# Kernel optimization log

Hardware: AMD Instinct MI355X
Metric: run time of the kernel (lower is better)

The kernel has to match this reference:

```python
import jax, jax.numpy as jnp
import numpy as np

N = 100000   # nodes
E = 1600000  # edges
P = 16       # num_properties
H = 64       # hidden_dim
EPS = 1e-12  # F.normalize eps


def _lin_params(key, din, dout):
    return (jax.random.normal(key, (din, dout), jnp.float32) / np.sqrt(din),
            jnp.zeros((dout,), jnp.float32))


def _mlp(x, W1, b1, W2, b2):
    # MLP(in, out, hidden_layers=[H]): Linear -> ReLU -> Linear
    return jnp.maximum(x @ W1 + b1, 0.0) @ W2 + b2


def setup_inputs() -> dict:
    key = jax.random.key(0)
    ks = jax.random.split(key, 12)
    h = jax.random.normal(ks[0], (N, P), jnp.float32)
    x = jax.random.normal(ks[1], (N, 3), jnp.float32)
    edge_index = jax.random.randint(ks[2], (2, E), 0, N, jnp.int64)
    emb_W, emb_b = _lin_params(ks[3], P, H)
    eW1, eb1 = _lin_params(ks[4], 2 * H + 1, H)
    eW2, eb2 = _lin_params(ks[5], H, H)
    nW1, nb1 = _lin_params(ks[6], 2 * H, H)
    nW2, nb2 = _lin_params(ks[7], H, H)
    wW1, wb1 = _lin_params(ks[8], H, H)
    wW2, wb2 = _lin_params(ks[9], H, 1)
    return {"h": h, "x": x, "edge_index": edge_index,
            "emb_W": emb_W, "emb_b": emb_b,
            "eW1": eW1, "eb1": eb1, "eW2": eW2, "eb2": eb2,
            "nW1": nW1, "nb1": nb1, "nW2": nW2, "nb2": nb2,
            "wW1": wW1, "wb1": wb1, "wW2": wW2, "wb2": wb2}


def reference(h, x, edge_index, emb_W, emb_b, eW1, eb1, eW2, eb2,
              nW1, nb1, nW2, nb2, wW1, wb1, wW2, wb2):
    row, col = edge_index[0], edge_index[1]
    h = h @ emb_W + emb_b  # [N,H] node embedding

    rel_pos = x[row] - x[col]                               # [E,3]
    rel_dist = jnp.sum(rel_pos ** 2, axis=-1, keepdims=True)  # [E,1]
    rel_theta = jnp.arctan2(rel_pos[:, 1], rel_pos[:, 0])
    rel_phi = jnp.arctan2(rel_pos[:, 2],
                          jnp.sqrt(rel_pos[:, 0] ** 2 + rel_pos[:, 1] ** 2))
    rel_pos_spin2 = rel_dist * jnp.stack(
        [jnp.cos(2 * rel_theta), jnp.sin(2 * rel_theta), rel_phi], axis=1)  # [E,3]

    # single layer (num_layers=1; original code only executable in this config)
    edge_inputs = jnp.concatenate([h[row], h[col], rel_dist], axis=-1)  # [E,2H+1]
    edge_feat = _mlp(edge_inputs, eW1, eb1, eW2, eb2)                   # [E,H]
    agg = jax.ops.segment_sum(edge_feat, row, num_segments=N)           # [N,H]
    h = h + _mlp(jnp.concatenate([h, agg], axis=-1), nW1, nb1, nW2, nb2)

    w = _mlp(edge_feat, wW1, wb1, wW2, wb2)              # [E,1]
    rel_scaled = rel_pos_spin2[:, None, :] * w[:, :, None]  # [E,1,3]
    v_sum = jax.ops.segment_sum(rel_scaled, row, num_segments=N)  # [N,1,3]
    cnt = jax.ops.segment_sum(jnp.ones((E,), jnp.float32), row, num_segments=N)
    v = v_sum / jnp.maximum(cnt, 1.0)[:, None, None]     # scatter-mean

    v = v[:, :2]  # slice along dim 1 (faithful to torch v[:, :2])
    norm = jnp.linalg.norm(v, axis=-1, keepdims=True)
    v = v / jnp.maximum(norm, EPS)  # F.normalize(p=2, dim=-1)
    return (h, x, v)
```

## Files before the change

kernel.cpp:

```cpp
#include <hip/hip_runtime.h>
#include <math.h>

#define NN 100000
#define EE 1600000
#define NBLK_SCAN 256
#define CHUNK ((NN + NBLK_SCAN - 1) / NBLK_SCAN)

typedef __attribute__((ext_vector_type(8))) short bf16x8;
typedef __attribute__((ext_vector_type(4))) float f32x4;

__device__ __forceinline__ ushort f2bf(float x) {
    uint u = __builtin_bit_cast(uint, x);
    u += 0x7fffu + ((u >> 16) & 1u);
    return (ushort)(u >> 16);
}
__device__ __forceinline__ float bf2f(ushort u) {
    uint v = ((uint)u) << 16;
    return __builtin_bit_cast(float, v);
}

__global__ __launch_bounds__(256) void embed_kernel(
    const float* __restrict__ h, const float* __restrict__ embW,
    const float* __restrict__ embB, ushort* __restrict__ hembb)
{
    int t = blockIdx.x * 256 + threadIdx.x;
    int n = t >> 6;
    int j = t & 63;
    if (n >= NN) return;
    float acc = embB[j];
#pragma unroll
    for (int k = 0; k < 16; ++k)
        acc = fmaf(h[n * 16 + k], embW[k * 64 + j], acc);
    hembb[n * 64 + j] = f2bf(acc);
}

__global__ __launch_bounds__(256) void hist_kernel(
    const int* __restrict__ ei, int* __restrict__ hist)
{
    for (int e = blockIdx.x * 256 + threadIdx.x; e < EE; e += gridDim.x * 256)
        atomicAdd(&hist[ei[e]], 1);
}

__global__ __launch_bounds__(256) void scan_a(const int* __restrict__ hist, int* __restrict__ bsum)
{
    __shared__ int red[256];
    const int b = blockIdx.x, t = threadIdx.x;
    const int start = b * CHUNK, end = min(NN, start + CHUNK);
    int s = 0;
    for (int i = start + t; i < end; i += 256) s += hist[i];
    red[t] = s; __syncthreads();
    for (int k = 128; k > 0; k >>= 1) { if (t < k) red[t] += red[t + k]; __syncthreads(); }
    if (t == 0) bsum[b] = red[0];
}

__global__ void scan_b(const int* __restrict__ bsum, int* __restrict__ boff)
{
    if (threadIdx.x == 0) {
        int acc = 0;
        for (int i = 0; i < NBLK_SCAN; ++i) { boff[i] = acc; acc += bsum[i]; }
    }
}

__global__ __launch_bounds__(256) void scan_c(
    const int* __restrict__ hist, const int* __restrict__ boff,
    int* __restrict__ csr, int* __restrict__ cursor)
{
    __shared__ int lds[CHUNK];
    const int b = blockIdx.x, t = threadIdx.x;
    const int start = b * CHUNK, end = min(NN, start + CHUNK), n = end - start;
    for (int i = t; i < n; i += 256) lds[i] = hist[start + i];
    __syncthreads();
    if (t == 0) {
        int acc = boff[b];
        for (int i = 0; i < n; ++i) { int v = lds[i]; lds[i] = acc; acc += v; }
        if (end == NN) csr[NN] = acc;
    }
    __syncthreads();
    for (int i = t; i < n; i += 256) { csr[start + i] = lds[i]; cursor[start + i] = lds[i]; }
}

__global__ __launch_bounds__(256) void scatter_kernel(
    const int* __restrict__ ei, int* __restrict__ cursor, int2* __restrict__ srt)
{
    for (int e = blockIdx.x * 256 + threadIdx.x; e < EE; e += gridDim.x * 256) {
        const int row = ei[e];
        const int p = atomicAdd(&cursor[row], 1);
        srt[p] = make_int2(row, ei[EE + e]);
    }
}

__global__ __launch_bounds__(512, 2) void edge_kernel(
    const ushort* __restrict__ hembb, const float* __restrict__ x,
    const int2* __restrict__ srt,
    const float* __restrict__ eW1, const float* __restrict__ eb1,
    const float* __restrict__ eW2, const float* __restrict__ eb2,
    const float* __restrict__ wW1, const float* __restrict__ wb1,
    const float* __restrict__ wW2, const float* __restrict__ wb2,
    float* __restrict__ agg, float* __restrict__ vsum)
{
    __shared__ ushort sS[8][2560];
    __shared__ float  sScal[8][16][4];

    const int tid = threadIdx.x;
    const int wave = tid >> 6, lane = tid & 63;
    const int l15 = lane & 15, g = lane >> 4;

    bf16x8 W1f[4][4], W2f[2][4], WVf[2][4];
#pragma unroll
    for (int kc = 0; kc < 4; ++kc)
#pragma unroll
        for (int t = 0; t < 4; ++t) {
            bf16x8 f;
#pragma unroll
            for (int b = 0; b < 8; ++b) {
                int k = kc * 32 + g * 8 + b;
                f[b] = (short)f2bf(eW1[k * 64 + t * 16 + l15]);
            }
            W1f[kc][t] = f;
        }
#pragma unroll
    for (int kc = 0; kc < 2; ++kc)
#pragma unroll
        for (int t = 0; t < 4; ++t) {
            bf16x8 f, fv;
#pragma unroll
            for (int b = 0; b < 8; ++b) {
                int s = kc * 32 + g * 8 + b;
                int j = (s >> 2) + (s & 3) * 16;
                f[b]  = (short)f2bf(eW2[j * 64 + t * 16 + l15]);
                fv[b] = (short)f2bf(wW1[j * 64 + t * 16 + l15]);
            }
            W2f[kc][t] = f; WVf[kc][t] = fv;
        }
    float b1v[4], b2v[4], wb1v[4], w2v[4], w128v[4];
#pragma unroll
    for (int t = 0; t < 4; ++t) {
        b1v[t]   = eb1[t * 16 + l15];
        b2v[t]   = eb2[t * 16 + l15];
        wb1v[t]  = wb1[t * 16 + l15];
        w2v[t]   = wW2[t * 16 + l15];
        w128v[t] = eW1[128 * 64 + t * 16 + l15];
    }
    const float wb2v = wb2[0];

    ushort* Xl = sS[wave];
    ushort* T1 = sS[wave];
    ushort* EF = sS[wave] + 1280;

    const int base = (blockIdx.x * 8 + wave) * 400;

    float carry = 0.f, carryv = 0.f;
    int cur_row = -1;

    for (int bt = 0; bt < 25; ++bt) {
        const int ebase = base + bt * 16;

        int rowv = 0, colv = 0;
        if (lane < 16) {
            const int2 rc = srt[ebase + lane];
            rowv = rc.x; colv = rc.y;
            const float dx = x[rowv * 3 + 0] - x[colv * 3 + 0];
            const float dy = x[rowv * 3 + 1] - x[colv * 3 + 1];
            const float dz = x[rowv * 3 + 2] - x[colv * 3 + 2];
            const float r2 = dx * dx + dy * dy;
            const float rdv = r2 + dz * dz;
            const float inv = (r2 > 0.f) ? (1.f / r2) : 0.f;
            const float c2  = (r2 > 0.f) ? ((dx * dx - dy * dy) * inv) : 1.f;
            const float sn2 = 2.f * dx * dy * inv;
            const float phi = atan2f(dz, sqrtf(r2));
            float4 sc = {rdv, rdv * c2, rdv * sn2, rdv * phi};
            *(float4*)&sScal[wave][lane][0] = sc;
        }

        uint gv[16];
#pragma unroll
        for (int e = 0; e < 16; ++e) {
            const int re = __shfl(rowv, e);
            const int ce = __shfl(colv, e);
            const int node = (lane < 32) ? re : ce;
            gv[e] = *(const uint*)&hembb[(size_t)node * 64 + (lane & 31) * 2];
        }
#pragma unroll
        for (int e = 0; e < 16; ++e)
            *(uint*)&Xl[e * 144 + (lane & 31) * 2 + ((lane < 32) ? 0 : 64)] = gv[e];

        f32x4 acc[4];
#pragma unroll
        for (int t = 0; t < 4; ++t) acc[t] = (f32x4){b1v[t], b1v[t], b1v[t], b1v[t]};
#pragma unroll
        for (int kc = 0; kc < 4; ++kc) {
            bf16x8 a = *(const bf16x8*)&Xl[l15 * 144 + kc * 32 + g * 8];
#pragma unroll
            for (int t = 0; t < 4; ++t)
                acc[t] = __builtin_amdgcn_mfma_f32_16x16x32_bf16(a, W1f[kc][t], acc[t], 0, 0, 0);
        }
#pragma unroll
        for (int r = 0; r < 4; ++r) {
            const float rd_r = sScal[wave][g * 4 + r][0];
#pragma unroll
            for (int t = 0; t < 4; ++t) acc[t][r] = fmaf(rd_r, w128v[t], acc[t][r]);
        }
#pragma unroll
        for (int r = 0; r < 4; ++r) {
            const float v0 = fmaxf(acc[0][r], 0.f), v1 = fmaxf(acc[1][r], 0.f);
            const float v2 = fmaxf(acc[2][r], 0.f), v3 = fmaxf(acc[3][r], 0.f);
            uint2 p;
            p.x = (uint)f2bf(v0) | ((uint)f2bf(v1) << 16);
            p.y = (uint)f2bf(v2) | ((uint)f2bf(v3) << 16);
            *(uint2*)&T1[(g * 4 + r) * 80 + l15 * 4] = p;
        }

        f32x4 acc2[4];
#pragma unroll
        for (int t = 0; t < 4; ++t) acc2[t] = (f32x4){b2v[t], b2v[t], b2v[t], b2v[t]};
#pragma unroll
        for (int kc = 0; kc < 2; ++kc) {
            bf16x8 a = *(const bf16x8*)&T1[l15 * 80 + kc * 32 + g * 8];
#pragma unroll
            for (int t = 0; t < 4; ++t)
                acc2[t] = __builtin_amdgcn_mfma_f32_16x16x32_bf16(a, W2f[kc][t], acc2[t], 0, 0, 0);
        }
#pragma unroll
        for (int r = 0; r < 4; ++r) {
            uint2 p;
            p.x = (uint)f2bf(acc2[0][r]) | ((uint)f2bf(acc2[1][r]) << 16);
            p.y = (uint)f2bf(acc2[2][r]) | ((uint)f2bf(acc2[3][r]) << 16);
            *(uint2*)&EF[(g * 4 + r) * 80 + l15 * 4] = p;
        }

        f32x4 acc3[4];
#pragma unroll
        for (int t = 0; t < 4; ++t) acc3[t] = (f32x4){wb1v[t], wb1v[t], wb1v[t], wb1v[t]};
#pragma unroll
        for (int kc = 0; kc < 2; ++kc) {
            bf16x8 a = *(const bf16x8*)&EF[l15 * 80 + kc * 32 + g * 8];
#pragma unroll
            for (int t = 0; t < 4; ++t)
                acc3[t] = __builtin_amdgcn_mfma_f32_16x16x32_bf16(a, WVf[kc][t], acc3[t], 0, 0, 0);
        }
        float wfin[4];
#pragma unroll
        for (int r = 0; r < 4; ++r) {
            float p = fmaxf(acc3[0][r], 0.f) * w2v[0];
            p = fmaf(fmaxf(acc3[1][r], 0.f), w2v[1], p);
            p = fmaf(fmaxf(acc3[2][r], 0.f), w2v[2], p);
            p = fmaf(fmaxf(acc3[3][r], 0.f), w2v[3], p);
            wfin[r] = p;
        }
#pragma unroll
        for (int m = 1; m < 16; m <<= 1) {
#pragma unroll
            for (int r = 0; r < 4; ++r) wfin[r] += __shfl_xor(wfin[r], m);
        }
#pragma unroll
        for (int r = 0; r < 4; ++r) wfin[r] += wb2v;

#pragma unroll
        for (int e = 0; e < 16; ++e) {
            const int row_e = __shfl(rowv, e);
            const float efv = bf2f(EF[e * 80 + l15 * 4 + g]);
            const float wE = __shfl(wfin[e & 3], (e >> 2) * 16);
            if (row_e != cur_row) {
                if (cur_row >= 0) {
                    unsafeAtomicAdd(&agg[(size_t)cur_row * 64 + lane], carry);
                    if (lane < 3) unsafeAtomicAdd(&vsum[cur_row * 4 + lane], carryv);
                }
                cur_row = row_e; carry = 0.f; carryv = 0.f;
            }
            carry += efv;
            if (lane < 3) carryv = fmaf(sScal[wave][e][1 + lane], wE, carryv);
        }
    }
    if (cur_row >= 0) {
        unsafeAtomicAdd(&agg[(size_t)cur_row * 64 + lane], carry);
        if (lane < 3) unsafeAtomicAdd(&vsum[cur_row * 4 + lane], carryv);
    }
}

__global__ __launch_bounds__(256, 2) void node_kernel(
    const ushort* __restrict__ hembb, const float* __restrict__ agg,
    const float* __restrict__ nW1, const float* __restrict__ nb1,
    const float* __restrict__ nW2, const float* __restrict__ nb2,
    const float* __restrict__ vsum, const int* __restrict__ csr,
    float* __restrict__ outh, float* __restrict__ outv)
{
    __shared__ ushort sT1[4][16 * 80];

    const int tid = threadIdx.x;
    const int wave = tid >> 6, lane = tid & 63;
    const int l15 = lane & 15, g = lane >> 4;

    bf16x8 W1f[4][4], W2f[2][4];
#pragma unroll
    for (int kc = 0; kc < 4; ++kc)
#pragma unroll
        for (int t = 0; t < 4; ++t) {
            bf16x8 f;
#pragma unroll
            for (int b = 0; b < 8; ++b) {
                int k = kc * 32 + g * 8 + b;
                f[b] = (short)f2bf(nW1[k * 64 + t * 16 + l15]);
            }
            W1f[kc][t] = f;
        }
#pragma unroll
    for (int kc = 0; kc < 2; ++kc)
#pragma unroll
        for (int t = 0; t < 4; ++t) {
            bf16x8 f;
#pragma unroll
            for (int b = 0; b < 8; ++b) {
                int s = kc * 32 + g * 8 + b;
                int j = (s >> 2) + (s & 3) * 16;
                f[b] = (short)f2bf(nW2[j * 64 + t * 16 + l15]);
            }
            W2f[kc][t] = f;
        }
    float b1v[4], b2v[4];
#pragma unroll
    for (int t = 0; t < 4; ++t) { b1v[t] = nb1[t * 16 + l15]; b2v[t] = nb2[t * 16 + l15]; }

    ushort* T1 = sT1[wave];
    const int nwaves = gridDim.x * 4;
    const int ntiles = NN / 16;

    for (int tile = blockIdx.x * 4 + wave; tile < ntiles; tile += nwaves) {
        const int nb = tile * 16;

        f32x4 acc[4];
#pragma unroll
        for (int t = 0; t < 4; ++t) acc[t] = (f32x4){b1v[t], b1v[t], b1v[t], b1v[t]};
#pragma unroll
        for (int kc = 0; kc < 2; ++kc) {
            bf16x8 a = *(const bf16x8*)&hembb[(size_t)(nb + l15) * 64 + kc * 32 + g * 8];
#pragma unroll
            for (int t = 0; t < 4; ++t)
                acc[t] = __builtin_amdgcn_mfma_f32_16x16x32_bf16(a, W1f[kc][t], acc[t], 0, 0, 0);
        }
#pragma unroll
        for (int kc = 2; kc < 4; ++kc) {
            const float4 f0 = *(const float4*)&agg[(size_t)(nb + l15) * 64 + (kc - 2) * 32 + g * 8];
            const float4 f1 = *(const float4*)&agg[(size_t)(nb + l15) * 64 + (kc - 2) * 32 + g * 8 + 4];
            bf16x8 a;
            a[0] = (short)f2bf(f0.x); a[1] = (short)f2bf(f0.y);
            a[2] = (short)f2bf(f0.z); a[3] = (short)f2bf(f0.w);
            a[4] = (short)f2bf(f1.x); a[5] = (short)f2bf(f1.y);
            a[6] = (short)f2bf(f1.z); a[7] = (short)f2bf(f1.w);
#pragma unroll
            for (int t = 0; t < 4; ++t)
                acc[t] = __builtin_amdgcn_mfma_f32_16x16x32_bf16(a, W1f[kc][t], acc[t], 0, 0, 0);
        }
#pragma unroll
        for (int r = 0; r < 4; ++r) {
            const float v0 = fmaxf(acc[0][r], 0.f), v1 = fmaxf(acc[1][r], 0.f);
            const float v2 = fmaxf(acc[2][r], 0.f), v3 = fmaxf(acc[3][r], 0.f);
            uint2 p;
            p.x = (uint)f2bf(v0) | ((uint)f2bf(v1) << 16);
            p.y = (uint)f2bf(v2) | ((uint)f2bf(v3) << 16);
            *(uint2*)&T1[(g * 4 + r) * 80 + l15 * 4] = p;
        }

        f32x4 acc2[4];
#pragma unroll
        for (int t = 0; t < 4; ++t) acc2[t] = (f32x4){b2v[t], b2v[t], b2v[t], b2v[t]};
#pragma unroll
        for (int kc = 0; kc < 2; ++kc) {
            bf16x8 a = *(const bf16x8*)&T1[l15 * 80 + kc * 32 + g * 8];
#pragma unroll
            for (int t = 0; t < 4; ++t)
                acc2[t] = __builtin_amdgcn_mfma_f32_16x16x32_bf16(a, W2f[kc][t], acc2[t], 0, 0, 0);
        }
#pragma unroll
        for (int r = 0; r < 4; ++r) {
#pragma unroll
            for (int t = 0; t < 4; ++t) {
                const size_t idx = (size_t)(nb + g * 4 + r) * 64 + t * 16 + l15;
                outh[idx] = bf2f(hembb[idx]) + acc2[t][r];
            }
        }

        if (g == 0) {
            const int n = nb + l15;
            const float c = fmaxf((float)(csr[n + 1] - csr[n]), 1.f);
            const float4 vs = *(const float4*)&vsum[n * 4];
            const float a0 = vs.x / c, a1 = vs.y / c, a2 = vs.z / c;
            const float nrm = fmaxf(sqrtf(a0 * a0 + a1 * a1 + a2 * a2), 1e-12f);
            outv[n * 3 + 0] = a0 / nrm;
            outv[n * 3 + 1] = a1 / nrm;
            outv[n * 3 + 2] = a2 / nrm;
        }
    }
}

extern "C" void kernel_launch(void* const* d_in, const int* in_sizes, int n_in,
                              void* d_out, int out_size, void* d_ws, size_t ws_size,
                              hipStream_t stream)
{
    const float* h    = (const float*)d_in[0];
    const float* x    = (const float*)d_in[1];
    const int*   ei   = (const int*)d_in[2];
    const float* embW = (const float*)d_in[3];
    const float* embB = (const float*)d_in[4];
    const float* eW1  = (const float*)d_in[5];
    const float* eb1  = (const float*)d_in[6];
    const float* eW2  = (const float*)d_in[7];
    const float* eb2  = (const float*)d_in[8];
    const float* nW1  = (const float*)d_in[9];
    const float* nb1  = (const float*)d_in[10];
    const float* nW2  = (const float*)d_in[11];
    const float* nb2  = (const float*)d_in[12];
    const float* wW1  = (const float*)d_in[13];
    const float* wb1  = (const float*)d_in[14];
    const float* wW2  = (const float*)d_in[15];
    const float* wb2  = (const float*)d_in[16];

    float* ws     = (float*)d_ws;
    ushort* hembb = (ushort*)ws;
    float* agg    = ws + (size_t)NN * 32;
    float* vsum   = agg + (size_t)NN * 64;
    int*   hist   = (int*)(vsum + (size_t)NN * 4);
    int*   csr    = hist + NN;
    int*   cursor = csr + NN + 1;
    int*   bsum   = cursor + NN;
    int*   boff   = bsum + NBLK_SCAN;
    int2*  srt    = (int2*)(boff + NBLK_SCAN);

    float* outh = (float*)d_out;
    float* outx = outh + (size_t)NN * 64;
    float* outv = outx + (size_t)NN * 3;

    hipMemsetAsync(agg, 0, ((size_t)NN * 64 + NN * 4 + NN) * sizeof(float), stream);

    embed_kernel<<<NN * 64 / 256, 256, 0, stream>>>(h, embW, embB, hembb);
    hipMemcpyAsync(outx, x, (size_t)NN * 3 * sizeof(float), hipMemcpyDeviceToDevice, stream);

    hist_kernel<<<2048, 256, 0, stream>>>(ei, hist);
    scan_a<<<NBLK_SCAN, 256, 0, stream>>>(hist, bsum);
    scan_b<<<1, 64, 0, stream>>>(bsum, boff);
    scan_c<<<NBLK_SCAN, 256, 0, stream>>>(hist, boff, csr, cursor);
    scatter_kernel<<<2048, 256, 0, stream>>>(ei, cursor, srt);

    edge_kernel<<<500, 512, 0, stream>>>(hembb, x, srt, eW1, eb1, eW2, eb2,
                                         wW1, wb1, wW2, wb2, agg, vsum);
    node_kernel<<<1563, 256, 0, stream>>>(hembb, agg, nW1, nb1, nW2, nb2,
                                          vsum, csr, outh, outv);
}
```

Baseline: 523.2 us.

## Move MFMA weight fragments to shared memory and gather embeddings directly into registers

Weight fragments for the three edge MLP matmuls are now built once per block into shared memory instead of being held in registers by every wave, and launch bounds are raised to allow four blocks per CU. The node embedding gather now loads bf16x8 A-fragments straight from global memory into registers, skipping the LDS staging round trip. This cuts register pressure so more waves can hide gather latency. In exchange every MFMA reads its weight operand from LDS, which adds LDS bandwidth pressure and a block-wide barrier at startup.

```diff
diff --git a/kernel.cpp b/kernel.cpp
--- a/kernel.cpp
+++ b/kernel.cpp
@@ -89,7 +89,7 @@
     }
 }
 
-__global__ __launch_bounds__(512, 2) void edge_kernel(
+__global__ __launch_bounds__(512, 4) void edge_kernel(
     const ushort* __restrict__ hembb, const float* __restrict__ x,
     const int2* __restrict__ srt,
     const float* __restrict__ eW1, const float* __restrict__ eb1,
@@ -98,6 +98,7 @@
     const float* __restrict__ wW2, const float* __restrict__ wb2,
     float* __restrict__ agg, float* __restrict__ vsum)
 {
+    __shared__ ushort sWB[32 * 512];
     __shared__ ushort sS[8][2560];
     __shared__ float  sScal[8][16][4];
 
@@ -105,33 +106,30 @@
     const int wave = tid >> 6, lane = tid & 63;
     const int l15 = lane & 15, g = lane >> 4;
 
-    bf16x8 W1f[4][4], W2f[2][4], WVf[2][4];
-#pragma unroll
-    for (int kc = 0; kc < 4; ++kc)
-#pragma unroll
-        for (int t = 0; t < 4; ++t) {
-            bf16x8 f;
-#pragma unroll
-            for (int b = 0; b < 8; ++b) {
-                int k = kc * 32 + g * 8 + b;
-                f[b] = (short)f2bf(eW1[k * 64 + t * 16 + l15]);
-            }
-            W1f[kc][t] = f;
-        }
-#pragma unroll
-    for (int kc = 0; kc < 2; ++kc)
-#pragma unroll
-        for (int t = 0; t < 4; ++t) {
-            bf16x8 f, fv;
-#pragma unroll
-            for (int b = 0; b < 8; ++b) {
-                int s = kc * 32 + g * 8 + b;
-                int j = (s >> 2) + (s & 3) * 16;
-                f[b]  = (short)f2bf(eW2[j * 64 + t * 16 + l15]);
-                fv[b] = (short)f2bf(wW1[j * 64 + t * 16 + l15]);
-            }
-            W2f[kc][t] = f; WVf[kc][t] = fv;
-        }
+#pragma unroll
+    for (int q = 0; q < 2; ++q) {
+        const int fi = wave * 2 + q;
+        const int kc = fi >> 2, t = fi & 3;
+        bf16x8 f;
+#pragma unroll
+        for (int b = 0; b < 8; ++b)
+            f[b] = (short)f2bf(eW1[(kc * 32 + g * 8 + b) * 64 + t * 16 + l15]);
+        *(bf16x8*)&sWB[fi * 512 + lane * 8] = f;
+    }
+    {
+        const int kc = wave >> 2, t = wave & 3;
+        bf16x8 f, fv;
+#pragma unroll
+        for (int b = 0; b < 8; ++b) {
+            int s = kc * 32 + g * 8 + b;
+            int j = (s >> 2) + (s & 3) * 16;
+            f[b]  = (short)f2bf(eW2[j * 64 + t * 16 + l15]);
+            fv[b] = (short)f2bf(wW1[j * 64 + t * 16 + l15]);
+        }
+        *(bf16x8*)&sWB[(16 + wave) * 512 + lane * 8] = f;
+        *(bf16x8*)&sWB[(24 + wave) * 512 + lane * 8] = fv;
+    }
+
     float b1v[4], b2v[4], wb1v[4], w2v[4], w128v[4];
 #pragma unroll
     for (int t = 0; t < 4; ++t) {
@@ -142,8 +140,8 @@
         w128v[t] = eW1[128 * 64 + t * 16 + l15];
     }
     const float wb2v = wb2[0];
-
-    ushort* Xl = sS[wave];
+    __syncthreads();
+
     ushort* T1 = sS[wave];
     ushort* EF = sS[wave] + 1280;
 
@@ -172,27 +170,26 @@
             *(float4*)&sScal[wave][lane][0] = sc;
         }
 
-        uint gv[16];
-#pragma unroll
-        for (int e = 0; e < 16; ++e) {
-            const int re = __shfl(rowv, e);
-            const int ce = __shfl(colv, e);
-            const int node = (lane < 32) ? re : ce;
-            gv[e] = *(const uint*)&hembb[(size_t)node * 64 + (lane & 31) * 2];
-        }
-#pragma unroll
-        for (int e = 0; e < 16; ++e)
-            *(uint*)&Xl[e * 144 + (lane & 31) * 2 + ((lane < 32) ? 0 : 64)] = gv[e];
+        const int rowN = __shfl(rowv, l15);
+        const int colN = __shfl(colv, l15);
+        const bf16x8 a0 = *(const bf16x8*)&hembb[(size_t)rowN * 64 + g * 8];
+        const bf16x8 a1 = *(const bf16x8*)&hembb[(size_t)rowN * 64 + 32 + g * 8];
+        const bf16x8 a2 = *(const bf16x8*)&hembb[(size_t)colN * 64 + g * 8];
+        const bf16x8 a3 = *(const bf16x8*)&hembb[(size_t)colN * 64 + 32 + g * 8];
 
         f32x4 acc[4];
 #pragma unroll
         for (int t = 0; t < 4; ++t) acc[t] = (f32x4){b1v[t], b1v[t], b1v[t], b1v[t]};
 #pragma unroll
-        for (int kc = 0; kc < 4; ++kc) {
-            bf16x8 a = *(const bf16x8*)&Xl[l15 * 144 + kc * 32 + g * 8];
-#pragma unroll
-            for (int t = 0; t < 4; ++t)
-                acc[t] = __builtin_amdgcn_mfma_f32_16x16x32_bf16(a, W1f[kc][t], acc[t], 0, 0, 0);
+        for (int t = 0; t < 4; ++t) {
+            acc[t] = __builtin_amdgcn_mfma_f32_16x16x32_bf16(
+                a0, *(const bf16x8*)&sWB[(0 * 4 + t) * 512 + lane * 8], acc[t], 0, 0, 0);
+            acc[t] = __builtin_amdgcn_mfma_f32_16x16x32_bf16(
+                a1, *(const bf16x8*)&sWB[(1 * 4 + t) * 512 + lane * 8], acc[t], 0, 0, 0);
+            acc[t] = __builtin_amdgcn_mfma_f32_16x16x32_bf16(
+                a2, *(const bf16x8*)&sWB[(2 * 4 + t) * 512 + lane * 8], acc[t], 0, 0, 0);
+            acc[t] = __builtin_amdgcn_mfma_f32_16x16x32_bf16(
+                a3, *(const bf16x8*)&sWB[(3 * 4 + t) * 512 + lane * 8], acc[t], 0, 0, 0);
         }
 #pragma unroll
         for (int r = 0; r < 4; ++r) {
@@ -218,7 +215,8 @@
             bf16x8 a = *(const bf16x8*)&T1[l15 * 80 + kc * 32 + g * 8];
 #pragma unroll
             for (int t = 0; t < 4; ++t)
-                acc2[t] = __builtin_amdgcn_mfma_f32_16x16x32_bf16(a, W2f[kc][t], acc2[t], 0, 0, 0);
+                acc2[t] = __builtin_amdgcn_mfma_f32_16x16x32_bf16(
+                    a, *(const bf16x8*)&sWB[(16 + kc * 4 + t) * 512 + lane * 8], acc2[t], 0, 0, 0);
         }
 #pragma unroll
         for (int r = 0; r < 4; ++r) {
@@ -236,7 +234,8 @@
             bf16x8 a = *(const bf16x8*)&EF[l15 * 80 + kc * 32 + g * 8];
 #pragma unroll
             for (int t = 0; t < 4; ++t)
-                acc3[t] = __builtin_amdgcn_mfma_f32_16x16x32_bf16(a, WVf[kc][t], acc3[t], 0, 0, 0);
+                acc3[t] = __builtin_amdgcn_mfma_f32_16x16x32_bf16(
+                    a, *(const bf16x8*)&sWB[(24 + kc * 4 + t) * 512 + lane * 8], acc3[t], 0, 0, 0);
         }
         float wfin[4];
 #pragma unroll
```

New measurement: 730.1 us. 1.4x slower.
